# Kernel tuning notes

Hardware: AMD Instinct MI355X
Metric: run time of the kernel (lower is better)

## Reference

```python
import jax, jax.numpy as jnp
import numpy as np

B, S, D, H = 2, 2048, 1024, 16
HD = D // H  # 64


def setup_inputs() -> dict:
    key = jax.random.key(0)
    ks = jax.random.split(key, 10)
    sc = 1.0 / np.sqrt(D)
    return {
        "decoder_hs": jax.random.normal(ks[0], (B, S, D), jnp.float32),
        "encoder_hs": jax.random.normal(ks[1], (B, S, D), jnp.float32),
        "Wq": jax.random.normal(ks[2], (D, D), jnp.float32) * sc,
        "bq": jax.random.normal(ks[3], (D,), jnp.float32) * 0.02,
        "Wk": jax.random.normal(ks[4], (D, D), jnp.float32) * sc,
        "bk": jax.random.normal(ks[5], (D,), jnp.float32) * 0.02,
        "Wv": jax.random.normal(ks[6], (D, D), jnp.float32) * sc,
        "bv": jax.random.normal(ks[7], (D,), jnp.float32) * 0.02,
        "Wp": jax.random.normal(ks[8], (D, D), jnp.float32) * sc,
        "bp": jax.random.normal(ks[9], (D,), jnp.float32) * 0.02,
    }


def reference(decoder_hs, encoder_hs, Wq, bq, Wk, bk, Wv, bv, Wp, bp):
    b, s, d = decoder_hs.shape
    # torch nn.Linear: y = x @ W.T + b, W is [out, in]
    q = decoder_hs @ Wq.T + bq
    k = encoder_hs @ Wk.T + bk
    v = encoder_hs @ Wv.T + bv
    # head split: [b, s, d] -> [b, h, s, hd]
    q = q.reshape(b, s, H, HD).transpose(0, 2, 1, 3)
    k = k.reshape(b, s, H, HD).transpose(0, 2, 1, 3)
    v = v.reshape(b, s, H, HD).transpose(0, 2, 1, 3)
    scale = 1.0 / np.sqrt(HD).astype(np.float32)
    att = jnp.einsum('bhqd,bhkd->bhqk', q, k) * scale
    att = jax.nn.softmax(att, axis=-1)
    y = jnp.einsum('bhqk,bhkd->bhqd', att, v)
    y = y.transpose(0, 2, 1, 3).reshape(b, s, d)
    return y @ Wp.T + bp
```

## Files before the change

### kernel.cpp

```cpp
#include <hip/hip_runtime.h>
#include <hip/hip_bf16.h>
#include <cstdint>
#include <cstddef>

#define BB 2
#define SS 2048
#define DD 1024
#define HH 16
#define HD 64

typedef __attribute__((ext_vector_type(8))) short bf16x8;
typedef __attribute__((ext_vector_type(4))) float f32x4;

#define GLL(g, l) __builtin_amdgcn_global_load_lds( \
    (const __attribute__((address_space(1))) void*)(g), \
    (__attribute__((address_space(3))) void*)(l), 16, 0, 0)

__device__ __forceinline__ short f2bf_fast(float f) {
    uint32_t u = __float_as_uint(f);
    u += 0x7FFF + ((u >> 16) & 1);
    return (short)(u >> 16);
}
__device__ __forceinline__ uint32_t pack_bf2(float a, float b) {
    uint32_t ua = __float_as_uint(a), ub = __float_as_uint(b);
    ua += 0x7FFF + ((ua >> 16) & 1);
    ub += 0x7FFF + ((ub >> 16) & 1);
    return (ua >> 16) | (ub & 0xFFFF0000u);
}
__device__ __forceinline__ bf16x8 cvt8(const float* __restrict__ p) {
    float4 a = *(const float4*)p;
    float4 b = *(const float4*)(p + 4);
    union { uint32_t d[4]; bf16x8 v; } r;
    r.d[0] = pack_bf2(a.x, a.y);
    r.d[1] = pack_bf2(a.z, a.w);
    r.d[2] = pack_bf2(b.x, b.y);
    r.d[3] = pack_bf2(b.z, b.w);
    return r.v;
}

__global__ __launch_bounds__(256) void cvt6_kernel(
    const float* __restrict__ s0, const float* __restrict__ s1,
    const float* __restrict__ s2, const float* __restrict__ s3,
    const float* __restrict__ s4, const float* __restrict__ s5,
    short* __restrict__ d0, short* __restrict__ d1, short* __restrict__ d2,
    short* __restrict__ d3, short* __restrict__ d4, short* __restrict__ d5)
{
    const int z = blockIdx.z;
    const float* s = (z == 0) ? s0 : (z == 1) ? s1 : (z == 2) ? s2
                   : (z == 3) ? s3 : (z == 4) ? s4 : s5;
    short* d = (z == 0) ? d0 : (z == 1) ? d1 : (z == 2) ? d2
             : (z == 3) ? d3 : (z == 4) ? d4 : d5;
    const int n8 = (z < 2) ? (BB * SS * DD / 8) : (DD * DD / 8);
    const int id = blockIdx.x * 256 + threadIdx.x;
    if (id >= n8) return;
    bf16x8 r = cvt8(s + (size_t)id * 8);
    *(uint4*)(d + (size_t)id * 8) = *(uint4*)&r;
}

template<int BF>
__global__ __launch_bounds__(256, 2) void qkv_gemm_kernel(
    const void* __restrict__ dec, const void* __restrict__ enc,
    const void* __restrict__ Wq, const void* __restrict__ Wk,
    const void* __restrict__ Wv,
    const float* __restrict__ bq, const float* __restrict__ bk,
    const float* __restrict__ bv,
    short* __restrict__ Qo, short* __restrict__ Ko, short* __restrict__ Vo)
{
    __shared__ short As[128 * 32];
    __shared__ short Bs[128 * 32];

    const int z = blockIdx.z;
    const void* Xv = (z == 0) ? dec : enc;
    const void* Wp_ = (z == 0) ? Wq : (z == 1) ? Wk : Wv;
    const float* bias = (z == 0) ? bq : (z == 1) ? bk : bv;
    short* Yo = (z == 0) ? Qo : (z == 1) ? Ko : Vo;

    const int t = threadIdx.x;
    const int lane = t & 63, wv = t >> 6;
    const int lr = lane & 15, quad = lane >> 4;
    const int wm = wv >> 1, wn = wv & 1;
    const int m0 = blockIdx.y * 128;
    const int n0 = blockIdx.x * 128;
    const int K = DD;

    f32x4 acc[4][4];
    #pragma unroll
    for (int i = 0; i < 4; i++)
        #pragma unroll
        for (int j = 0; j < 4; j++) acc[i][j] = (f32x4){0.f, 0.f, 0.f, 0.f};

    for (int kb = 0; kb < K; kb += 32) {
        __syncthreads();
        if (BF) {
            const short* Xb = (const short*)Xv;
            const short* Wb = (const short*)Wp_;
            #pragma unroll
            for (int c = 0; c < 2; c++) {
                int r0 = wv * 32 + c * 16;
                int r = r0 + (lane >> 2), ch = (lane & 3) * 8;
                GLL(Xb + (size_t)(m0 + r) * K + kb + ch, &As[r0 * 32]);
                GLL(Wb + (size_t)(n0 + r) * K + kb + ch, &Bs[r0 * 32]);
            }
        } else {
            const float* Xf = (const float*)Xv;
            const float* Wf = (const float*)Wp_;
            #pragma unroll
            for (int c = 0; c < 2; c++) {
                int id = t + c * 256;
                int r = id >> 2, c8 = (id & 3) * 8;
                *(bf16x8*)&As[r * 32 + c8] = cvt8(Xf + (size_t)(m0 + r) * K + kb + c8);
                *(bf16x8*)&Bs[r * 32 + c8] = cvt8(Wf + (size_t)(n0 + r) * K + kb + c8);
            }
        }
        __syncthreads();

        bf16x8 af[4], bfr[4];
        #pragma unroll
        for (int mi = 0; mi < 4; mi++)
            af[mi] = *(const bf16x8*)&As[(wm * 64 + mi * 16 + lr) * 32 + quad * 8];
        #pragma unroll
        for (int ni = 0; ni < 4; ni++)
            bfr[ni] = *(const bf16x8*)&Bs[(wn * 64 + ni * 16 + lr) * 32 + quad * 8];
        #pragma unroll
        for (int mi = 0; mi < 4; mi++)
            #pragma unroll
            for (int ni = 0; ni < 4; ni++)
                acc[mi][ni] = __builtin_amdgcn_mfma_f32_16x16x32_bf16(
                    af[mi], bfr[ni], acc[mi][ni], 0, 0, 0);
    }

    #pragma unroll
    for (int ni = 0; ni < 4; ni++) {
        int col = n0 + wn * 64 + ni * 16 + lr;
        int h = col >> 6, hd = col & 63;
        float bvv = bias[col];
        #pragma unroll
        for (int mi = 0; mi < 4; mi++) {
            #pragma unroll
            for (int r2 = 0; r2 < 4; r2++) {
                int row = m0 + wm * 64 + mi * 16 + quad * 4 + r2;
                int b = row >> 11, s = row & 2047;
                float v = acc[mi][ni][r2] + bvv;
                size_t off;
                if (z < 2)
                    off = ((size_t)(b * HH + h) * SS + s) * HD + hd;
                else
                    off = ((size_t)(b * HH + h) * HD + hd) * SS + s;
                Yo[off] = f2bf_fast(v);
            }
        }
    }
}

template<int WBF>
__global__ __launch_bounds__(256, 2) void proj_gemm_kernel(
    const short* __restrict__ X,
    const void* __restrict__ W, const float* __restrict__ bias,
    float* __restrict__ Y)
{
    __shared__ short As[64 * 32];
    __shared__ short Bs[128 * 32];

    const int t = threadIdx.x;
    const int lane = t & 63, wv = t >> 6;
    const int lr = lane & 15, quad = lane >> 4;
    const int wm = wv >> 1, wn = wv & 1;
    const int m0 = blockIdx.y * 64;
    const int n0 = blockIdx.x * 128;
    const int K = DD, N = DD;

    f32x4 acc[2][4];
    #pragma unroll
    for (int i = 0; i < 2; i++)
        #pragma unroll
        for (int j = 0; j < 4; j++) acc[i][j] = (f32x4){0.f, 0.f, 0.f, 0.f};

    for (int kb = 0; kb < K; kb += 32) {
        __syncthreads();
        {
            int r0 = wv * 16;
            int r = r0 + (lane >> 2), ch = (lane & 3) * 8;
            GLL(X + (size_t)(m0 + r) * K + kb + ch, &As[r0 * 32]);
        }
        if (WBF) {
            const short* Wb = (const short*)W;
            #pragma unroll
            for (int c = 0; c < 2; c++) {
                int r0 = wv * 32 + c * 16;
                int r = r0 + (lane >> 2), ch = (lane & 3) * 8;
                GLL(Wb + (size_t)(n0 + r) * K + kb + ch, &Bs[r0 * 32]);
            }
        } else {
            const float* Wf = (const float*)W;
            #pragma unroll
            for (int c = 0; c < 2; c++) {
                int id = t + c * 256;
                int r = id >> 2, c8 = (id & 3) * 8;
                *(bf16x8*)&Bs[r * 32 + c8] = cvt8(Wf + (size_t)(n0 + r) * K + kb + c8);
            }
        }
        __syncthreads();

        bf16x8 af[2], bfr[4];
        #pragma unroll
        for (int mi = 0; mi < 2; mi++)
            af[mi] = *(const bf16x8*)&As[(wm * 32 + mi * 16 + lr) * 32 + quad * 8];
        #pragma unroll
        for (int ni = 0; ni < 4; ni++)
            bfr[ni] = *(const bf16x8*)&Bs[(wn * 64 + ni * 16 + lr) * 32 + quad * 8];
        #pragma unroll
        for (int mi = 0; mi < 2; mi++)
            #pragma unroll
            for (int ni = 0; ni < 4; ni++)
                acc[mi][ni] = __builtin_amdgcn_mfma_f32_16x16x32_bf16(
                    af[mi], bfr[ni], acc[mi][ni], 0, 0, 0);
    }

    #pragma unroll
    for (int ni = 0; ni < 4; ni++) {
        int col = n0 + wn * 64 + ni * 16 + lr;
        float bvv = bias[col];
        #pragma unroll
        for (int mi = 0; mi < 2; mi++) {
            #pragma unroll
            for (int r2 = 0; r2 < 4; r2++) {
                int row = m0 + wm * 32 + mi * 16 + quad * 4 + r2;
                Y[(size_t)row * N + col] = acc[mi][ni][r2] + bvv;
            }
        }
    }
}

__global__ __launch_bounds__(256, 2) void attn_kernel(
    const short* __restrict__ Q,
    const short* __restrict__ Kgl,
    const short* __restrict__ Vt_g,
    short* __restrict__ Y)
{
    __shared__ short Ks[128][72];
    __shared__ short Vt[64][136];
    __shared__ short Ps[4][16][136];

    const int t = threadIdx.x;
    const int lane = t & 63, w = t >> 6;
    const int lr = lane & 15, quad = lane >> 4;

    const int qt = blockIdx.x & 31;
    const int bh = blockIdx.x >> 5;
    const int b = bh >> 4, h = bh & 15;

    const float C = 0.125f * 1.44269504088896f;

    const short* Qp = Q + ((size_t)bh * SS + qt * 64 + w * 16 + lr) * HD;
    bf16x8 qf[2];
    qf[0] = *(const bf16x8*)(Qp + quad * 8);
    qf[1] = *(const bf16x8*)(Qp + 32 + quad * 8);

    bf16x8 ones;
    #pragma unroll
    for (int j = 0; j < 8; j++) ones[j] = (short)0x3F80;

    f32x4 o[4], lacc;
    #pragma unroll
    for (int i = 0; i < 4; i++) o[i] = (f32x4){0.f, 0.f, 0.f, 0.f};
    lacc = (f32x4){0.f, 0.f, 0.f, 0.f};

    const uint4* Kg0 = (const uint4*)(Kgl + (size_t)bh * SS * HD);
    const short* Vg0 = Vt_g + (size_t)bh * HD * SS;

    for (int kt = 0; kt < SS / 128; kt++) {
        __syncthreads();
        const uint4* Kg = Kg0 + (size_t)kt * 128 * 8;
        #pragma unroll
        for (int c = 0; c < 4; c++) {
            int id = t + c * 256;
            int row = id >> 3, h8 = id & 7;
            *(uint4*)&Ks[row][h8 * 8] = Kg[id];
        }
        #pragma unroll
        for (int c = 0; c < 4; c++) {
            int id = t + c * 256;
            int hd = id >> 4, s16 = id & 15;
            *(uint4*)&Vt[hd][s16 * 8] =
                *(const uint4*)(Vg0 + (size_t)hd * SS + kt * 128 + s16 * 8);
        }
        __syncthreads();

        f32x4 sc[8];
        #pragma unroll
        for (int nt = 0; nt < 8; nt++) {
            sc[nt] = (f32x4){0.f, 0.f, 0.f, 0.f};
            bf16x8 kf0 = *(const bf16x8*)&Ks[nt * 16 + lr][quad * 8];
            bf16x8 kf1 = *(const bf16x8*)&Ks[nt * 16 + lr][32 + quad * 8];
            sc[nt] = __builtin_amdgcn_mfma_f32_16x16x32_bf16(qf[0], kf0, sc[nt], 0, 0, 0);
            sc[nt] = __builtin_amdgcn_mfma_f32_16x16x32_bf16(qf[1], kf1, sc[nt], 0, 0, 0);
        }

        #pragma unroll
        for (int r2 = 0; r2 < 4; r2++) {
            #pragma unroll
            for (int nt = 0; nt < 8; nt++) {
                float p = __builtin_amdgcn_exp2f(sc[nt][r2] * C);
                Ps[w][quad * 4 + r2][nt * 16 + lr] = f2bf_fast(p);
            }
        }

        bf16x8 pa[4];
        #pragma unroll
        for (int kf = 0; kf < 4; kf++)
            pa[kf] = *(const bf16x8*)&Ps[w][lr][kf * 32 + quad * 8];
        #pragma unroll
        for (int kf = 0; kf < 4; kf++)
            lacc = __builtin_amdgcn_mfma_f32_16x16x32_bf16(pa[kf], ones, lacc, 0, 0, 0);
        #pragma unroll
        for (int nt = 0; nt < 4; nt++) {
            #pragma unroll
            for (int kf = 0; kf < 4; kf++) {
                bf16x8 vb = *(const bf16x8*)&Vt[nt * 16 + lr][kf * 32 + quad * 8];
                o[nt] = __builtin_amdgcn_mfma_f32_16x16x32_bf16(pa[kf], vb, o[nt], 0, 0, 0);
            }
        }
    }

    #pragma unroll
    for (int r2 = 0; r2 < 4; r2++) {
        float inv = 1.0f / lacc[r2];
        int srow = qt * 64 + w * 16 + quad * 4 + r2;
        #pragma unroll
        for (int nt = 0; nt < 4; nt++) {
            size_t off = ((size_t)b * SS + srow) * DD + h * 64 + nt * 16 + lr;
            Y[off] = f2bf_fast(o[nt][r2] * inv);
        }
    }
}

extern "C" void kernel_launch(void* const* d_in, const int* in_sizes, int n_in,
                              void* d_out, int out_size, void* d_ws, size_t ws_size,
                              hipStream_t stream) {
    const float* dec = (const float*)d_in[0];
    const float* enc = (const float*)d_in[1];
    const float* Wq  = (const float*)d_in[2];
    const float* bq  = (const float*)d_in[3];
    const float* Wk  = (const float*)d_in[4];
    const float* bk  = (const float*)d_in[5];
    const float* Wv  = (const float*)d_in[6];
    const float* bv  = (const float*)d_in[7];
    const float* Wp  = (const float*)d_in[8];
    const float* bp  = (const float*)d_in[9];

    const size_t per = (size_t)BB * HH * SS * HD;
    const size_t wsz = (size_t)DD * DD;
    short* ws = (short*)d_ws;
    short* Qb  = ws;
    short* Kb  = ws + per;
    short* Vtb = ws + 2 * per;
    short* Yb  = ws + 3 * per;

    dim3 qkv_grid(DD / 128, (BB * SS) / 128, 3);
    dim3 proj_grid(DD / 128, (BB * SS) / 64);
    const int attn_blocks = BB * HH * (SS / 64);

    const size_t need = (6 * per + 4 * wsz) * sizeof(short);
    if (ws_size >= need) {
        short* decb = ws + 4 * per;
        short* encb = ws + 5 * per;
        short* Wqb  = ws + 6 * per;
        short* Wkb  = Wqb + wsz;
        short* Wvb  = Wqb + 2 * wsz;
        short* Wpb  = Wqb + 3 * wsz;
        cvt6_kernel<<<dim3((BB * SS * DD / 8 + 255) / 256, 1, 6), 256, 0, stream>>>(
            dec, enc, Wq, Wk, Wv, Wp, decb, encb, Wqb, Wkb, Wvb, Wpb);
        qkv_gemm_kernel<1><<<qkv_grid, 256, 0, stream>>>(
            decb, encb, Wqb, Wkb, Wvb, bq, bk, bv, Qb, Kb, Vtb);
        attn_kernel<<<attn_blocks, 256, 0, stream>>>(Qb, Kb, Vtb, Yb);
        proj_gemm_kernel<1><<<proj_grid, 256, 0, stream>>>(Yb, Wpb, bp, (float*)d_out);
    } else {
        qkv_gemm_kernel<0><<<qkv_grid, 256, 0, stream>>>(
            dec, enc, Wq, Wk, Wv, bq, bk, bv, Qb, Kb, Vtb);
        attn_kernel<<<attn_blocks, 256, 0, stream>>>(Qb, Kb, Vtb, Yb);
        proj_gemm_kernel<0><<<proj_grid, 256, 0, stream>>>(Yb, Wp, bp, (float*)d_out);
    }
}
```

Baseline: 238.1 us.

## Keep softmax probabilities in registers via transposed QK^T and 16x16x16 MFMA for PV

Computes S^T by swapping the MFMA operands, so each lane holds probabilities in the layout the 16x16x16 bf16 MFMA expects as its B operand. That removes the LDS round trip for P and the ones-vector MFMA used for row sums, which are now accumulated in registers and reduced with shuffles. Output stores are packed into 8-byte writes. Launch bounds are raised for the attention and QKV kernels to allow more waves per CU. The price is more, smaller MFMAs for PV and a risk of register spills under the tighter occupancy bounds.

```diff
diff --git a/kernel.cpp b/kernel.cpp
--- a/kernel.cpp
+++ b/kernel.cpp
@@ -10,7 +10,10 @@
 #define HD 64
 
 typedef __attribute__((ext_vector_type(8))) short bf16x8;
+typedef __attribute__((ext_vector_type(4))) short bf16x4;
 typedef __attribute__((ext_vector_type(4))) float f32x4;
+
+#define MFMA16(va, vb, c) __builtin_amdgcn_mfma_f32_16x16x16bf16_1k(va, vb, c, 0, 0, 0)
 
 #define GLL(g, l) __builtin_amdgcn_global_load_lds( \
     (const __attribute__((address_space(1))) void*)(g), \
@@ -58,7 +61,7 @@
 }
 
 template<int BF>
-__global__ __launch_bounds__(256, 2) void qkv_gemm_kernel(
+__global__ __launch_bounds__(256, 3) void qkv_gemm_kernel(
     const void* __restrict__ dec, const void* __restrict__ enc,
     const void* __restrict__ Wq, const void* __restrict__ Wk,
     const void* __restrict__ Wv,
@@ -231,7 +234,7 @@
     }
 }
 
-__global__ __launch_bounds__(256, 2) void attn_kernel(
+__global__ __launch_bounds__(256, 4) void attn_kernel(
     const short* __restrict__ Q,
     const short* __restrict__ Kgl,
     const short* __restrict__ Vt_g,
@@ -239,7 +242,6 @@
 {
     __shared__ short Ks[128][72];
     __shared__ short Vt[64][136];
-    __shared__ short Ps[4][16][136];
 
     const int t = threadIdx.x;
     const int lane = t & 63, w = t >> 6;
@@ -252,18 +254,13 @@
     const float C = 0.125f * 1.44269504088896f;
 
     const short* Qp = Q + ((size_t)bh * SS + qt * 64 + w * 16 + lr) * HD;
-    bf16x8 qf[2];
-    qf[0] = *(const bf16x8*)(Qp + quad * 8);
-    qf[1] = *(const bf16x8*)(Qp + 32 + quad * 8);
-
-    bf16x8 ones;
-    #pragma unroll
-    for (int j = 0; j < 8; j++) ones[j] = (short)0x3F80;
-
-    f32x4 o[4], lacc;
+    bf16x8 qf0 = *(const bf16x8*)(Qp + quad * 8);
+    bf16x8 qf1 = *(const bf16x8*)(Qp + 32 + quad * 8);
+
+    f32x4 o[4];
     #pragma unroll
     for (int i = 0; i < 4; i++) o[i] = (f32x4){0.f, 0.f, 0.f, 0.f};
-    lacc = (f32x4){0.f, 0.f, 0.f, 0.f};
+    float lsum = 0.f;
 
     const uint4* Kg0 = (const uint4*)(Kgl + (size_t)bh * SS * HD);
     const short* Vg0 = Vt_g + (size_t)bh * HD * SS;
@@ -289,48 +286,49 @@
         f32x4 sc[8];
         #pragma unroll
         for (int nt = 0; nt < 8; nt++) {
-            sc[nt] = (f32x4){0.f, 0.f, 0.f, 0.f};
             bf16x8 kf0 = *(const bf16x8*)&Ks[nt * 16 + lr][quad * 8];
             bf16x8 kf1 = *(const bf16x8*)&Ks[nt * 16 + lr][32 + quad * 8];
-            sc[nt] = __builtin_amdgcn_mfma_f32_16x16x32_bf16(qf[0], kf0, sc[nt], 0, 0, 0);
-            sc[nt] = __builtin_amdgcn_mfma_f32_16x16x32_bf16(qf[1], kf1, sc[nt], 0, 0, 0);
-        }
-
-        #pragma unroll
-        for (int r2 = 0; r2 < 4; r2++) {
+            sc[nt] = __builtin_amdgcn_mfma_f32_16x16x32_bf16(
+                kf0, qf0, (f32x4){0.f, 0.f, 0.f, 0.f}, 0, 0, 0);
+            sc[nt] = __builtin_amdgcn_mfma_f32_16x16x32_bf16(kf1, qf1, sc[nt], 0, 0, 0);
+        }
+
+        bf16x4 pb[8];
+        #pragma unroll
+        for (int nt = 0; nt < 8; nt++) {
+            float p0 = __builtin_amdgcn_exp2f(sc[nt][0] * C);
+            float p1 = __builtin_amdgcn_exp2f(sc[nt][1] * C);
+            float p2 = __builtin_amdgcn_exp2f(sc[nt][2] * C);
+            float p3 = __builtin_amdgcn_exp2f(sc[nt][3] * C);
+            lsum += (p0 + p1) + (p2 + p3);
+            union { uint32_t d[2]; bf16x4 v; } u;
+            u.d[0] = pack_bf2(p0, p1);
+            u.d[1] = pack_bf2(p2, p3);
+            pb[nt] = u.v;
+        }
+
+        #pragma unroll
+        for (int dt = 0; dt < 4; dt++) {
             #pragma unroll
             for (int nt = 0; nt < 8; nt++) {
-                float p = __builtin_amdgcn_exp2f(sc[nt][r2] * C);
-                Ps[w][quad * 4 + r2][nt * 16 + lr] = f2bf_fast(p);
-            }
-        }
-
-        bf16x8 pa[4];
-        #pragma unroll
-        for (int kf = 0; kf < 4; kf++)
-            pa[kf] = *(const bf16x8*)&Ps[w][lr][kf * 32 + quad * 8];
-        #pragma unroll
-        for (int kf = 0; kf < 4; kf++)
-            lacc = __builtin_amdgcn_mfma_f32_16x16x32_bf16(pa[kf], ones, lacc, 0, 0, 0);
-        #pragma unroll
-        for (int nt = 0; nt < 4; nt++) {
-            #pragma unroll
-            for (int kf = 0; kf < 4; kf++) {
-                bf16x8 vb = *(const bf16x8*)&Vt[nt * 16 + lr][kf * 32 + quad * 8];
-                o[nt] = __builtin_amdgcn_mfma_f32_16x16x32_bf16(pa[kf], vb, o[nt], 0, 0, 0);
-            }
-        }
-    }
-
-    #pragma unroll
-    for (int r2 = 0; r2 < 4; r2++) {
-        float inv = 1.0f / lacc[r2];
-        int srow = qt * 64 + w * 16 + quad * 4 + r2;
-        #pragma unroll
-        for (int nt = 0; nt < 4; nt++) {
-            size_t off = ((size_t)b * SS + srow) * DD + h * 64 + nt * 16 + lr;
-            Y[off] = f2bf_fast(o[nt][r2] * inv);
-        }
+                bf16x4 va = *(const bf16x4*)&Vt[dt * 16 + lr][nt * 16 + quad * 4];
+                o[dt] = MFMA16(va, pb[nt], o[dt]);
+            }
+        }
+    }
+
+    lsum += __shfl_xor(lsum, 16, 64);
+    lsum += __shfl_xor(lsum, 32, 64);
+    float inv = 1.0f / lsum;
+
+    const int srow = qt * 64 + w * 16 + lr;
+    short* Yp = Y + ((size_t)b * SS + srow) * DD + h * 64 + quad * 4;
+    #pragma unroll
+    for (int dt = 0; dt < 4; dt++) {
+        union { uint32_t d[2]; } u;
+        u.d[0] = pack_bf2(o[dt][0] * inv, o[dt][1] * inv);
+        u.d[1] = pack_bf2(o[dt][2] * inv, o[dt][3] * inv);
+        *(uint2*)(Yp + dt * 16) = *(uint2*)&u;
     }
 }
 
```

Result: no change. 240.7 us (+1.1%).
